# Kernel optimization log

Measured on AMD Instinct MI355X. Metric: run time of the kernel, lower is better.

## Reference

```python
import jax, jax.numpy as jnp
import numpy as np
import math

D_MODEL = 64
X_KS = 32   # input_kernel_size
Y_KS = 32   # output_kernel_size
HIDDEN = 256


def pos_enc(pos, d_model=D_MODEL):
    # standard interleaved sinusoidal encoding indexed by integer position
    i = jnp.arange(d_model // 2, dtype=jnp.float32)
    inv_freq = jnp.power(jnp.float32(10000.0), -(2.0 * i) / d_model)
    ang = pos.astype(jnp.float32)[:, None] * inv_freq[None, :]      # [N, d/2]
    pe = jnp.stack([jnp.sin(ang), jnp.cos(ang)], axis=-1)           # [N, d/2, 2]
    return pe.reshape(pos.shape[0], d_model)


def setup_inputs() -> dict:
    key = jax.random.key(0)
    ks = jax.random.split(key, 9)
    B, IN = 64, 1024
    d_in_w = 2 * D_MODEL + X_KS   # 160
    d_in_b = D_MODEL + Y_KS       # 96
    def lin(k, fan_in, fan_out):
        s = 1.0 / math.sqrt(fan_in)
        return jax.random.uniform(k, (fan_in, fan_out), jnp.float32, -s, s)
    return {
        "x": jax.random.normal(ks[0], (B, IN), jnp.float32),
        "output_size": 1024,
        "W1": lin(ks[1], d_in_w, HIDDEN), "b1": jnp.zeros((HIDDEN,), jnp.float32),
        "W2": lin(ks[2], HIDDEN, X_KS * Y_KS), "b2": jnp.zeros((X_KS * Y_KS,), jnp.float32),
        "Wb1": lin(ks[3], d_in_b, HIDDEN), "bb1": jnp.zeros((HIDDEN,), jnp.float32),
        "Wb2": lin(ks[4], HIDDEN, Y_KS), "bb2": jnp.zeros((Y_KS,), jnp.float32),
    }


def reference(x, output_size, W1, b1, W2, b2, Wb1, bb1, Wb2, bb2):
    B, input_size = x.shape
    gen_x = math.ceil(output_size / Y_KS)
    gen_y = math.ceil(input_size / X_KS)

    # pad x up to gen_y*X_KS and chunk into kernel windows, tiled gen_x times
    new_x = jnp.pad(x, ((0, 0), (0, gen_y * X_KS - input_size)))
    new_x = new_x.reshape(B, gen_y, X_KS)
    new_x = jnp.tile(new_x, (1, gen_x, 1))                          # [B, gx*gy, X_KS]

    arg_x = jnp.tile(jnp.arange(gen_x), gen_y)                      # [gx*gy]
    arg_y = jnp.repeat(jnp.arange(gen_y), gen_x)                    # [gx*gy]
    pe_x = jnp.broadcast_to(pos_enc(arg_x)[None], (B, gen_x * gen_y, D_MODEL))
    pe_y = jnp.broadcast_to(pos_enc(arg_y)[None], (B, gen_x * gen_y, D_MODEL))

    argument = jnp.concatenate([pe_x, pe_y, new_x], axis=2)         # [B, G, 2d+X_KS]

    # hypernetwork generates per-sample weight matrix
    h = jnp.tanh(argument @ W1 + b1)
    w = h @ W2 + b2                                                 # [B, G, X_KS*Y_KS]
    weight = w.reshape(B, gen_y * X_KS, gen_x * Y_KS)[:, :input_size, :output_size]

    out = jnp.einsum("bi,bio->bo", x, weight)                       # [B, output_size]

    # bias hypernetwork
    out_pad = jnp.pad(out, ((0, 0), (0, gen_x * Y_KS - output_size)))
    out_pad = out_pad.reshape(B, gen_x, Y_KS)
    pe_b = jnp.broadcast_to(pos_enc(jnp.arange(gen_x))[None], (B, gen_x, D_MODEL))
    hb = jnp.tanh(jnp.concatenate([out_pad, pe_b], axis=2) @ Wb1 + bb1)
    bias = (hb @ Wb2 + bb2).reshape(B, -1)[:, :output_size]

    return out + bias
```

## Files before the change

### kernel.cpp

```cpp
#include <hip/hip_runtime.h>
#include <math.h>

constexpr int B    = 64;
constexpr int IN   = 1024;
constexpr int OUTN = 1024;
constexpr int H    = 256;

#define LN10000 9.210340371976184f
#define TWO_LOG2E 2.8853900817779268f

__device__ __forceinline__ float fast_tanh(float x) {
    x = fminf(fmaxf(x, -15.0f), 15.0f);
    float e = __builtin_amdgcn_exp2f(x * TWO_LOG2E);
    return 1.0f - 2.0f * __builtin_amdgcn_rcpf(e + 1.0f);
}

__global__ void __launch_bounds__(512) k1_v(const float* __restrict__ x,
                                            const float* __restrict__ W1,
                                            const float* __restrict__ b1,
                                            float* __restrict__ v,
                                            float* __restrict__ S) {
    __shared__ float xs[1024];
    __shared__ float pe[32 * 64];
    __shared__ float A[32 * 64];
    __shared__ float Pyl[32 * 64];
    __shared__ float red[512];
    const int blk = blockIdx.x, tid = threadIdx.x;
    const int b = blk >> 2, cq = blk & 3, c0 = cq * 64;

    ((float2*)xs)[tid] = ((const float2*)(x + b * IN))[tid];
    #pragma unroll
    for (int r = 0; r < 2; ++r) {
        const int idx = r * 512 + tid;
        const int p = idx >> 5, i = idx & 31;
        float freq = expf(-(2.0f * (float)i / 64.0f) * LN10000);
        float a = (float)p * freq;
        pe[p * 64 + 2 * i]     = sinf(a);
        pe[p * 64 + 2 * i + 1] = cosf(a);
    }
    __syncthreads();

    if (cq == 0) {
        red[tid] = xs[tid] + xs[tid + 512];
        __syncthreads();
        for (int s = 256; s > 0; s >>= 1) {
            if (tid < s) red[tid] += red[tid + s];
            __syncthreads();
        }
        if (tid == 0) S[b] = red[0];
    }

    const int cl = tid & 63, jg = tid >> 6, j0 = jg * 4;
    const float b1v = b1[c0 + cl];
    float accA[4], accP[4];
    #pragma unroll
    for (int r = 0; r < 4; ++r) { accA[r] = b1v; accP[r] = 0.0f; }
    for (int d = 0; d < 64; ++d) {
        const float wx = W1[d * H + c0 + cl];
        const float wy = W1[(64 + d) * H + c0 + cl];
        #pragma unroll
        for (int r = 0; r < 4; ++r) {
            const float p = pe[(j0 + r) * 64 + d];
            accA[r] += p * wx;
            accP[r] += p * wy;
        }
    }
    for (int k = 0; k < 32; ++k) {
        const float wq = W1[(128 + k) * H + c0 + cl];
        #pragma unroll
        for (int r = 0; r < 4; ++r) accA[r] += xs[(j0 + r) * 32 + k] * wq;
    }
    #pragma unroll
    for (int r = 0; r < 4; ++r) {
        A[(j0 + r) * 64 + cl]   = accA[r];
        Pyl[(j0 + r) * 64 + cl] = accP[r];
    }
    __syncthreads();

    float Areg[32];
    #pragma unroll
    for (int jx = 0; jx < 32; ++jx) Areg[jx] = A[jx * 64 + cl];
    float acc = 0.0f;
    for (int r = 0; r < 4; ++r) {
        const int jy = j0 + r;
        const float pyv = Pyl[jy * 64 + cl];
        const float4* xr = (const float4*)(xs + jy * 32);
        #pragma unroll
        for (int q = 0; q < 8; ++q) {
            float4 xv = xr[q];
            acc += xv.x * fast_tanh(Areg[q * 4 + 0] + pyv);
            acc += xv.y * fast_tanh(Areg[q * 4 + 1] + pyv);
            acc += xv.z * fast_tanh(Areg[q * 4 + 2] + pyv);
            acc += xv.w * fast_tanh(Areg[q * 4 + 3] + pyv);
        }
    }
    red[tid] = acc;
    __syncthreads();
    if (tid < 64) {
        float s = 0.0f;
        #pragma unroll
        for (int g = 0; g < 8; ++g) s += red[g * 64 + tid];
        v[b * H + c0 + tid] = s;
    }
}

__global__ void __launch_bounds__(256) k2_out(const float* __restrict__ v,
                                              const float* __restrict__ S,
                                              const float* __restrict__ W2,
                                              const float* __restrict__ b2,
                                              const float* __restrict__ Wb1,
                                              const float* __restrict__ bb1,
                                              const float* __restrict__ Wb2,
                                              const float* __restrict__ bb2,
                                              float* __restrict__ out) {
    __shared__ float vsh[8 * 256];
    __shared__ float pes[64];
    __shared__ float hpe[256];
    __shared__ float os[8 * 32];
    __shared__ float hbs[8 * 256];
    __shared__ float Ssh[8];
    const int blk = blockIdx.x, tid = threadIdx.x;
    const int og = blk & 31, bg = blk >> 5;
    const int bl = tid >> 5, ol = tid & 31;
    const int b0 = bg * 8;

    ((float4*)vsh)[tid]       = ((const float4*)(v + b0 * H))[tid];
    ((float4*)vsh)[tid + 256] = ((const float4*)(v + b0 * H))[tid + 256];
    if (tid < 8) Ssh[tid] = S[b0 + tid];
    if (tid >= 64 && tid < 96) {
        const int i = tid - 64;
        float freq = expf(-(2.0f * (float)i / 64.0f) * LN10000);
        float a = (float)og * freq;
        pes[2 * i]     = sinf(a);
        pes[2 * i + 1] = cosf(a);
    }
    __syncthreads();

    {
        float a = bb1[tid];
        #pragma unroll 8
        for (int d = 0; d < 64; ++d)
            a += pes[d] * Wb1[(32 + d) * H + tid];
        hpe[tid] = a;
    }

    const int o = og * 32 + ol;
    float acc = Ssh[bl] * b2[o];
    const float4* vr = (const float4*)(vsh + bl * 256);
    #pragma unroll 4
    for (int c4 = 0; c4 < 64; ++c4) {
        float4 v4 = vr[c4];
        acc += v4.x * W2[(c4 * 4 + 0) * OUTN + o];
        acc += v4.y * W2[(c4 * 4 + 1) * OUTN + o];
        acc += v4.z * W2[(c4 * 4 + 2) * OUTN + o];
        acc += v4.w * W2[(c4 * 4 + 3) * OUTN + o];
    }
    os[bl * 32 + ol] = acc;
    __syncthreads();

    {
        const int c8 = ol * 8;
        float a[8];
        #pragma unroll
        for (int j = 0; j < 8; ++j) a[j] = hpe[c8 + j];
        #pragma unroll 4
        for (int k = 0; k < 32; ++k) {
            const float xo = os[bl * 32 + k];
            const float4* wr = (const float4*)(Wb1 + k * H + c8);
            float4 w0 = wr[0], w1 = wr[1];
            a[0] += xo * w0.x; a[1] += xo * w0.y; a[2] += xo * w0.z; a[3] += xo * w0.w;
            a[4] += xo * w1.x; a[5] += xo * w1.y; a[6] += xo * w1.z; a[7] += xo * w1.w;
        }
        #pragma unroll
        for (int j = 0; j < 8; ++j) hbs[bl * 256 + c8 + j] = fast_tanh(a[j]);
    }
    __syncthreads();

    {
        float bias = bb2[ol];
        const float4* hr = (const float4*)(hbs + bl * 256);
        #pragma unroll 4
        for (int c4 = 0; c4 < 64; ++c4) {
            float4 h4 = hr[c4];
            bias += h4.x * Wb2[(c4 * 4 + 0) * 32 + ol];
            bias += h4.y * Wb2[(c4 * 4 + 1) * 32 + ol];
            bias += h4.z * Wb2[(c4 * 4 + 2) * 32 + ol];
            bias += h4.w * Wb2[(c4 * 4 + 3) * 32 + ol];
        }
        out[(b0 + bl) * OUTN + og * 32 + ol] = os[bl * 32 + ol] + bias;
    }
}

extern "C" void kernel_launch(void* const* d_in, const int* in_sizes, int n_in,
                              void* d_out, int out_size, void* d_ws, size_t ws_size,
                              hipStream_t stream) {
    const float* x   = (const float*)d_in[0];
    const float* W1  = (const float*)d_in[2];
    const float* b1  = (const float*)d_in[3];
    const float* W2  = (const float*)d_in[4];
    const float* b2  = (const float*)d_in[5];
    const float* Wb1 = (const float*)d_in[6];
    const float* bb1 = (const float*)d_in[7];
    const float* Wb2 = (const float*)d_in[8];
    const float* bb2 = (const float*)d_in[9];
    float* out = (float*)d_out;

    float* v = (float*)d_ws;
    float* S = v + B * H;

    hipLaunchKernelGGL(k1_v,   dim3(B * 4), dim3(512), 0, stream, x, W1, b1, v, S);
    hipLaunchKernelGGL(k2_out, dim3(256),   dim3(256), 0, stream,
                       v, S, W2, b2, Wb1, bb1, Wb2, bb2, out);
}
```

Measured before the change: 103.1 us.

## Precompute positional-encoding tables in a prologue kernel and widen blocks to 1024 threads

Adds a small kernel that computes the batch-independent positional-encoding projections through W1, W1 (y part) and Wb1 once into workspace tables. The main kernels now run with 1024 threads per block. They read these tables instead of recomputing sin/cos and the 64-deep projections per block, and they split the W2 and Wb2 reductions across four thread groups with a shared-memory combine. This removes redundant per-block work and raises parallelism, at the cost of an extra kernel launch, more shared memory and extra syncs. The old path is kept as a fallback when the workspace is too small.

```diff
diff --git a/kernel.cpp b/kernel.cpp
--- a/kernel.cpp
+++ b/kernel.cpp
@@ -15,11 +15,197 @@
     return 1.0f - 2.0f * __builtin_amdgcn_rcpf(e + 1.0f);
 }
 
-__global__ void __launch_bounds__(512) k1_v(const float* __restrict__ x,
-                                            const float* __restrict__ W1,
-                                            const float* __restrict__ b1,
-                                            float* __restrict__ v,
-                                            float* __restrict__ S) {
+
+__global__ void __launch_bounds__(256) k0_tables(const float* __restrict__ W1,
+                                                 const float* __restrict__ b1,
+                                                 const float* __restrict__ Wb1,
+                                                 const float* __restrict__ bb1,
+                                                 float* __restrict__ PA,
+                                                 float* __restrict__ PY,
+                                                 float* __restrict__ HPE) {
+    __shared__ float pe[64];
+    const int blk = blockIdx.x, tid = threadIdx.x;
+    const int p = blk & 31, table = blk >> 5;
+    if (tid < 32) {
+        float freq = expf(-(2.0f * (float)tid / 64.0f) * LN10000);
+        float a = (float)p * freq;
+        pe[2 * tid]     = sinf(a);
+        pe[2 * tid + 1] = cosf(a);
+    }
+    __syncthreads();
+    const float* src; float bias; float* dst;
+    if (table == 0)      { src = W1;           bias = b1[tid];  dst = PA;  }
+    else if (table == 1) { src = W1 + 64 * H;  bias = 0.0f;     dst = PY;  }
+    else                 { src = Wb1 + 32 * H; bias = bb1[tid]; dst = HPE; }
+    float acc = bias;
+    #pragma unroll 16
+    for (int d = 0; d < 64; ++d) acc += pe[d] * src[d * H + tid];
+    dst[p * H + tid] = acc;
+}
+
+__global__ void __launch_bounds__(1024, 4) k1_new(const float* __restrict__ x,
+                                                  const float* __restrict__ W1,
+                                                  const float* __restrict__ PA,
+                                                  const float* __restrict__ PY,
+                                                  float* __restrict__ v,
+                                                  float* __restrict__ S) {
+    __shared__ float xs[1024];
+    __shared__ float w1s[2048];
+    __shared__ float As[2048];
+    __shared__ float Ps[2048];
+    __shared__ float red[1024];
+    const int blk = blockIdx.x, tid = threadIdx.x;
+    const int b = blk >> 2, cq = blk & 3, c0 = cq * 64;
+    const int cl = tid & 63, jg = tid >> 6;
+
+    xs[tid] = x[b * IN + tid];
+    #pragma unroll
+    for (int i = 0; i < 2; ++i) {
+        const int idx = i * 1024 + tid;
+        const int p = idx >> 6, c = idx & 63;
+        w1s[idx] = W1[(128 + p) * H + c0 + c];
+        Ps[idx]  = PY[p * H + c0 + c];
+    }
+    __syncthreads();
+
+    if (cq == 0 && tid < 64) {
+        float s = 0.0f;
+        #pragma unroll
+        for (int i = 0; i < 16; ++i) s += xs[tid + i * 64];
+        #pragma unroll
+        for (int off = 32; off > 0; off >>= 1) s += __shfl_xor(s, off, 64);
+        if (tid == 0) S[b] = s;
+    }
+
+    #pragma unroll
+    for (int r = 0; r < 2; ++r) {
+        const int jx = jg * 2 + r;
+        float q = PA[jx * H + c0 + cl];
+        #pragma unroll 8
+        for (int k = 0; k < 32; ++k)
+            q += xs[jx * 32 + k] * w1s[k * 64 + cl];
+        As[jx * 64 + cl] = q;
+    }
+    __syncthreads();
+
+    float Areg[32];
+    #pragma unroll
+    for (int jx = 0; jx < 32; ++jx) Areg[jx] = As[jx * 64 + cl];
+    float acc = 0.0f;
+    #pragma unroll
+    for (int r = 0; r < 2; ++r) {
+        const int jy = jg * 2 + r;
+        const float pyv = Ps[jy * 64 + cl];
+        const float4* xr = (const float4*)(xs + jy * 32);
+        #pragma unroll
+        for (int q8 = 0; q8 < 8; ++q8) {
+            float4 xv = xr[q8];
+            acc += xv.x * fast_tanh(Areg[q8 * 4 + 0] + pyv);
+            acc += xv.y * fast_tanh(Areg[q8 * 4 + 1] + pyv);
+            acc += xv.z * fast_tanh(Areg[q8 * 4 + 2] + pyv);
+            acc += xv.w * fast_tanh(Areg[q8 * 4 + 3] + pyv);
+        }
+    }
+    red[tid] = acc;
+    __syncthreads();
+    if (tid < 64) {
+        float s = 0.0f;
+        #pragma unroll
+        for (int g = 0; g < 16; ++g) s += red[g * 64 + tid];
+        v[b * H + c0 + tid] = s;
+    }
+}
+
+__global__ void __launch_bounds__(1024) k2_new(const float* __restrict__ v,
+                                               const float* __restrict__ S,
+                                               const float* __restrict__ W2,
+                                               const float* __restrict__ b2,
+                                               const float* __restrict__ Wb1,
+                                               const float* __restrict__ HPE,
+                                               const float* __restrict__ Wb2,
+                                               const float* __restrict__ bb2,
+                                               float* __restrict__ out) {
+    __shared__ float vsh[2048];
+    __shared__ float hpe[256];
+    __shared__ float osp[1024];
+    __shared__ float os[256];
+    __shared__ float hbs[2048];
+    __shared__ float Wb2s[8192];
+    __shared__ float bp[1024];
+    __shared__ float Ssh[8];
+    const int blk = blockIdx.x, tid = threadIdx.x;
+    const int og = blk & 31, bg = blk >> 5, b0 = bg * 8;
+    const int h = tid >> 8, u = tid & 255, bl = u >> 5, ol = u & 31;
+
+    ((float2*)vsh)[tid] = ((const float2*)(v + b0 * H))[tid];
+    #pragma unroll
+    for (int i = 0; i < 2; ++i)
+        ((float4*)Wb2s)[i * 1024 + tid] = ((const float4*)Wb2)[i * 1024 + tid];
+    if (tid < 256) hpe[tid] = HPE[og * H + tid];
+    if (tid < 8) Ssh[tid] = S[b0 + tid];
+    __syncthreads();
+
+    const int o = og * 32 + ol;
+    {
+        float acc = (h == 0) ? Ssh[bl] * b2[o] : 0.0f;
+        const float4* vr = (const float4*)(vsh + bl * H + h * 64);
+        const int cb = h * 64;
+        #pragma unroll
+        for (int c4 = 0; c4 < 16; ++c4) {
+            float4 v4 = vr[c4];
+            const int c = cb + c4 * 4;
+            acc += v4.x * W2[(c + 0) * OUTN + o];
+            acc += v4.y * W2[(c + 1) * OUTN + o];
+            acc += v4.z * W2[(c + 2) * OUTN + o];
+            acc += v4.w * W2[(c + 3) * OUTN + o];
+        }
+        osp[h * 256 + u] = acc;
+    }
+    __syncthreads();
+    if (tid < 256)
+        os[tid] = osp[tid] + osp[256 + tid] + osp[512 + tid] + osp[768 + tid];
+    __syncthreads();
+    {
+        float a0 = hpe[h * 64 + ol];
+        float a1 = hpe[h * 64 + 32 + ol];
+        #pragma unroll 8
+        for (int k = 0; k < 32; ++k) {
+            const float xo = os[bl * 32 + k];
+            const float* wr = Wb1 + k * H + h * 64 + ol;
+            a0 += xo * wr[0];
+            a1 += xo * wr[32];
+        }
+        hbs[bl * H + h * 64 + ol]      = fast_tanh(a0);
+        hbs[bl * H + h * 64 + 32 + ol] = fast_tanh(a1);
+    }
+    __syncthreads();
+    {
+        float bias = (h == 0) ? bb2[ol] : 0.0f;
+        const float4* hr = (const float4*)(hbs + bl * H + h * 64);
+        const int cb = h * 64;
+        #pragma unroll
+        for (int c4 = 0; c4 < 16; ++c4) {
+            float4 h4 = hr[c4];
+            const int c = cb + c4 * 4;
+            bias += h4.x * Wb2s[(c + 0) * 32 + ol];
+            bias += h4.y * Wb2s[(c + 1) * 32 + ol];
+            bias += h4.z * Wb2s[(c + 2) * 32 + ol];
+            bias += h4.w * Wb2s[(c + 3) * 32 + ol];
+        }
+        bp[h * 256 + u] = bias;
+    }
+    __syncthreads();
+    if (tid < 256) {
+        out[(b0 + (tid >> 5)) * OUTN + og * 32 + (tid & 31)] =
+            os[tid] + bp[tid] + bp[256 + tid] + bp[512 + tid] + bp[768 + tid];
+    }
+}
+
+__global__ void __launch_bounds__(512) k1_old(const float* __restrict__ x,
+                                              const float* __restrict__ W1,
+                                              const float* __restrict__ b1,
+                                              float* __restrict__ v,
+                                              float* __restrict__ S) {
     __shared__ float xs[1024];
     __shared__ float pe[32 * 64];
     __shared__ float A[32 * 64];
@@ -104,7 +290,7 @@
     }
 }
 
-__global__ void __launch_bounds__(256) k2_out(const float* __restrict__ v,
+__global__ void __launch_bounds__(256) k2_old(const float* __restrict__ v,
                                               const float* __restrict__ S,
                                               const float* __restrict__ W2,
                                               const float* __restrict__ b2,
@@ -208,7 +394,20 @@
     float* v = (float*)d_ws;
     float* S = v + B * H;
 
-    hipLaunchKernelGGL(k1_v,   dim3(B * 4), dim3(512), 0, stream, x, W1, b1, v, S);
-    hipLaunchKernelGGL(k2_out, dim3(256),   dim3(256), 0, stream,
-                       v, S, W2, b2, Wb1, bb1, Wb2, bb2, out);
-}
+    const size_t needA = (size_t)(B * H + B + 3 * 32 * H) * sizeof(float);
+    if (ws_size >= needA) {
+        float* PA  = S + B;
+        float* PY  = PA + 32 * H;
+        float* HPE = PY + 32 * H;
+        hipLaunchKernelGGL(k0_tables, dim3(96),  dim3(256),  0, stream,
+                           W1, b1, Wb1, bb1, PA, PY, HPE);
+        hipLaunchKernelGGL(k1_new,    dim3(B*4), dim3(1024), 0, stream,
+                           x, W1, PA, PY, v, S);
+        hipLaunchKernelGGL(k2_new,    dim3(256), dim3(1024), 0, stream,
+                           v, S, W2, b2, Wb1, HPE, Wb2, bb2, out);
+    } else {
+        hipLaunchKernelGGL(k1_old, dim3(B*4), dim3(512), 0, stream, x, W1, b1, v, S);
+        hipLaunchKernelGGL(k2_old, dim3(256), dim3(256), 0, stream,
+                           v, S, W2, b2, Wb1, bb1, Wb2, bb2, out);
+    }
+}
```

Result: faster. 90.96 us (-11.8%).

## Precompute positional-encoding tables once and widen k1/k2 to 1024 threads

Applied to the files above, without the earlier changes.

Adds a small pre-kernel that computes the positional-encoding projections through W1 (PA including b1, and PY) once, instead of every one of the 256 k1 blocks recomputing the full 32x64x64 pe products. k1 now uses 1024 threads, each holding one x element and broadcasting it through wavefront shuffles, with W1's x-rows kept in registers. k2 splits the hidden-dimension reductions across four thread groups with shared-memory partial sums to raise parallelism. The cost is an extra kernel launch, more workspace traffic, and extra synchronisation and reduction steps.

```diff
diff --git a/kernel.cpp b/kernel.cpp
--- a/kernel.cpp
+++ b/kernel.cpp
@@ -15,179 +15,180 @@
     return 1.0f - 2.0f * __builtin_amdgcn_rcpf(e + 1.0f);
 }
 
-__global__ void __launch_bounds__(512) k1_v(const float* __restrict__ x,
-                                            const float* __restrict__ W1,
-                                            const float* __restrict__ b1,
-                                            float* __restrict__ v,
-                                            float* __restrict__ S) {
-    __shared__ float xs[1024];
-    __shared__ float pe[32 * 64];
-    __shared__ float A[32 * 64];
-    __shared__ float Pyl[32 * 64];
-    __shared__ float red[512];
+__global__ void __launch_bounds__(256) k0_tables(const float* __restrict__ W1,
+                                                 const float* __restrict__ b1,
+                                                 float* __restrict__ PA,
+                                                 float* __restrict__ PY) {
+    __shared__ float pe[64];
+    const int blk = blockIdx.x, tid = threadIdx.x;
+    const int p = blk & 31, table = blk >> 5;
+    if (tid < 32) {
+        float freq = expf(-(2.0f * (float)tid / 64.0f) * LN10000);
+        float a = (float)p * freq;
+        pe[2 * tid]     = sinf(a);
+        pe[2 * tid + 1] = cosf(a);
+    }
+    __syncthreads();
+    const float* src = (table == 0) ? W1 : (W1 + 64 * H);
+    float acc = (table == 0) ? b1[tid] : 0.0f;
+    #pragma unroll 16
+    for (int d = 0; d < 64; ++d) acc += pe[d] * src[d * H + tid];
+    float* dst = (table == 0) ? PA : PY;
+    dst[p * H + tid] = acc;
+}
+
+__global__ void __launch_bounds__(1024, 4) k1_v(const float* __restrict__ x,
+                                                const float* __restrict__ W1,
+                                                const float* __restrict__ PA,
+                                                const float* __restrict__ PY,
+                                                float* __restrict__ v,
+                                                float* __restrict__ S) {
+    __shared__ float As[2048];
+    __shared__ float red[1024];
+    __shared__ float sred[16];
     const int blk = blockIdx.x, tid = threadIdx.x;
     const int b = blk >> 2, cq = blk & 3, c0 = cq * 64;
-
-    ((float2*)xs)[tid] = ((const float2*)(x + b * IN))[tid];
-    #pragma unroll
-    for (int r = 0; r < 2; ++r) {
-        const int idx = r * 512 + tid;
-        const int p = idx >> 5, i = idx & 31;
-        float freq = expf(-(2.0f * (float)i / 64.0f) * LN10000);
-        float a = (float)p * freq;
-        pe[p * 64 + 2 * i]     = sinf(a);
-        pe[p * 64 + 2 * i + 1] = cosf(a);
-    }
-    __syncthreads();
+    const int cl = tid & 63, jg = tid >> 6;
+    const int p0 = jg * 2;
+
+    const float xr = x[b * IN + tid];
+    float w1reg[32];
+    #pragma unroll
+    for (int k = 0; k < 32; ++k) w1reg[k] = W1[(128 + k) * H + c0 + cl];
+    float acc0 = PA[p0 * H + c0 + cl];
+    float acc1 = PA[(p0 + 1) * H + c0 + cl];
+    const float py0 = PY[p0 * H + c0 + cl];
+    const float py1 = PY[(p0 + 1) * H + c0 + cl];
 
     if (cq == 0) {
-        red[tid] = xs[tid] + xs[tid + 512];
-        __syncthreads();
-        for (int s = 256; s > 0; s >>= 1) {
-            if (tid < s) red[tid] += red[tid + s];
-            __syncthreads();
-        }
-        if (tid == 0) S[b] = red[0];
-    }
-
-    const int cl = tid & 63, jg = tid >> 6, j0 = jg * 4;
-    const float b1v = b1[c0 + cl];
-    float accA[4], accP[4];
-    #pragma unroll
-    for (int r = 0; r < 4; ++r) { accA[r] = b1v; accP[r] = 0.0f; }
-    for (int d = 0; d < 64; ++d) {
-        const float wx = W1[d * H + c0 + cl];
-        const float wy = W1[(64 + d) * H + c0 + cl];
-        #pragma unroll
-        for (int r = 0; r < 4; ++r) {
-            const float p = pe[(j0 + r) * 64 + d];
-            accA[r] += p * wx;
-            accP[r] += p * wy;
-        }
-    }
-    for (int k = 0; k < 32; ++k) {
-        const float wq = W1[(128 + k) * H + c0 + cl];
-        #pragma unroll
-        for (int r = 0; r < 4; ++r) accA[r] += xs[(j0 + r) * 32 + k] * wq;
-    }
-    #pragma unroll
-    for (int r = 0; r < 4; ++r) {
-        A[(j0 + r) * 64 + cl]   = accA[r];
-        Pyl[(j0 + r) * 64 + cl] = accP[r];
-    }
-    __syncthreads();
-
-    float Areg[32];
-    #pragma unroll
-    for (int jx = 0; jx < 32; ++jx) Areg[jx] = A[jx * 64 + cl];
+        float s = xr;
+        #pragma unroll
+        for (int off = 32; off > 0; off >>= 1) s += __shfl_xor(s, off, 64);
+        if (cl == 0) sred[jg] = s;
+    }
+
+    #pragma unroll
+    for (int k = 0; k < 32; ++k) acc0 += __shfl(xr, k, 64) * w1reg[k];
+    #pragma unroll
+    for (int k = 0; k < 32; ++k) acc1 += __shfl(xr, 32 + k, 64) * w1reg[k];
+
+    As[p0 * 64 + cl]       = acc0;
+    As[(p0 + 1) * 64 + cl] = acc1;
+    __syncthreads();
+
+    if (cq == 0 && tid == 0) {
+        float s = 0.0f;
+        #pragma unroll
+        for (int g = 0; g < 16; ++g) s += sred[g];
+        S[b] = s;
+    }
+
     float acc = 0.0f;
-    for (int r = 0; r < 4; ++r) {
-        const int jy = j0 + r;
-        const float pyv = Pyl[jy * 64 + cl];
-        const float4* xr = (const float4*)(xs + jy * 32);
-        #pragma unroll
-        for (int q = 0; q < 8; ++q) {
-            float4 xv = xr[q];
-            acc += xv.x * fast_tanh(Areg[q * 4 + 0] + pyv);
-            acc += xv.y * fast_tanh(Areg[q * 4 + 1] + pyv);
-            acc += xv.z * fast_tanh(Areg[q * 4 + 2] + pyv);
-            acc += xv.w * fast_tanh(Areg[q * 4 + 3] + pyv);
-        }
+    #pragma unroll
+    for (int jx = 0; jx < 32; ++jx) {
+        const float a = As[jx * 64 + cl];
+        acc += __shfl(xr, jx, 64)      * fast_tanh(a + py0);
+        acc += __shfl(xr, 32 + jx, 64) * fast_tanh(a + py1);
     }
     red[tid] = acc;
     __syncthreads();
     if (tid < 64) {
         float s = 0.0f;
         #pragma unroll
-        for (int g = 0; g < 8; ++g) s += red[g * 64 + tid];
+        for (int g = 0; g < 16; ++g) s += red[g * 64 + tid];
         v[b * H + c0 + tid] = s;
     }
 }
 
-__global__ void __launch_bounds__(256) k2_out(const float* __restrict__ v,
-                                              const float* __restrict__ S,
-                                              const float* __restrict__ W2,
-                                              const float* __restrict__ b2,
-                                              const float* __restrict__ Wb1,
-                                              const float* __restrict__ bb1,
-                                              const float* __restrict__ Wb2,
-                                              const float* __restrict__ bb2,
-                                              float* __restrict__ out) {
-    __shared__ float vsh[8 * 256];
-    __shared__ float pes[64];
+__global__ void __launch_bounds__(1024) k2_out(const float* __restrict__ v,
+                                               const float* __restrict__ S,
+                                               const float* __restrict__ W2,
+                                               const float* __restrict__ b2,
+                                               const float* __restrict__ Wb1,
+                                               const float* __restrict__ bb1,
+                                               const float* __restrict__ Wb2,
+                                               const float* __restrict__ bb2,
+                                               float* __restrict__ out) {
+    __shared__ float vsh[2048];
     __shared__ float hpe[256];
-    __shared__ float os[8 * 32];
-    __shared__ float hbs[8 * 256];
+    __shared__ float osp[1024];
+    __shared__ float os[256];
+    __shared__ float hbs[2048];
+    __shared__ float bp[1024];
     __shared__ float Ssh[8];
     const int blk = blockIdx.x, tid = threadIdx.x;
-    const int og = blk & 31, bg = blk >> 5;
-    const int bl = tid >> 5, ol = tid & 31;
-    const int b0 = bg * 8;
-
-    ((float4*)vsh)[tid]       = ((const float4*)(v + b0 * H))[tid];
-    ((float4*)vsh)[tid + 256] = ((const float4*)(v + b0 * H))[tid + 256];
+    const int og = blk & 31, bg = blk >> 5, b0 = bg * 8;
+    const int h = tid >> 8, u = tid & 255, bl = u >> 5, ol = u & 31;
+
+    ((float2*)vsh)[tid] = ((const float2*)(v + b0 * H))[tid];
     if (tid < 8) Ssh[tid] = S[b0 + tid];
-    if (tid >= 64 && tid < 96) {
-        const int i = tid - 64;
-        float freq = expf(-(2.0f * (float)i / 64.0f) * LN10000);
+    if (tid < 256) {
+        const int L = tid & 63;
+        float freq = expf(-(2.0f * (float)(L >> 1) / 64.0f) * LN10000);
         float a = (float)og * freq;
-        pes[2 * i]     = sinf(a);
-        pes[2 * i + 1] = cosf(a);
-    }
-    __syncthreads();
-
+        float pel = (L & 1) ? cosf(a) : sinf(a);
+        float accp = bb1[tid];
+        #pragma unroll 16
+        for (int d = 0; d < 64; ++d)
+            accp += __shfl(pel, d, 64) * Wb1[(32 + d) * H + tid];
+        hpe[tid] = accp;
+    }
+    __syncthreads();
+
+    const int o = og * 32 + ol;
     {
-        float a = bb1[tid];
-        #pragma unroll 8
-        for (int d = 0; d < 64; ++d)
-            a += pes[d] * Wb1[(32 + d) * H + tid];
-        hpe[tid] = a;
-    }
-
-    const int o = og * 32 + ol;
-    float acc = Ssh[bl] * b2[o];
-    const float4* vr = (const float4*)(vsh + bl * 256);
-    #pragma unroll 4
-    for (int c4 = 0; c4 < 64; ++c4) {
-        float4 v4 = vr[c4];
-        acc += v4.x * W2[(c4 * 4 + 0) * OUTN + o];
-        acc += v4.y * W2[(c4 * 4 + 1) * OUTN + o];
-        acc += v4.z * W2[(c4 * 4 + 2) * OUTN + o];
-        acc += v4.w * W2[(c4 * 4 + 3) * OUTN + o];
-    }
-    os[bl * 32 + ol] = acc;
-    __syncthreads();
-
+        float acc = (h == 0) ? Ssh[bl] * b2[o] : 0.0f;
+        const float4* vr = (const float4*)(vsh + bl * H + h * 64);
+        #pragma unroll
+        for (int c4 = 0; c4 < 16; ++c4) {
+            float4 v4 = vr[c4];
+            const int c = h * 64 + c4 * 4;
+            acc += v4.x * W2[(c + 0) * OUTN + o];
+            acc += v4.y * W2[(c + 1) * OUTN + o];
+            acc += v4.z * W2[(c + 2) * OUTN + o];
+            acc += v4.w * W2[(c + 3) * OUTN + o];
+        }
+        osp[h * 256 + u] = acc;
+    }
+    __syncthreads();
+    if (tid < 256)
+        os[tid] = osp[tid] + osp[256 + tid] + osp[512 + tid] + osp[768 + tid];
+    __syncthreads();
     {
-        const int c8 = ol * 8;
-        float a[8];
-        #pragma unroll
-        for (int j = 0; j < 8; ++j) a[j] = hpe[c8 + j];
-        #pragma unroll 4
-        for (int k = 0; k < 32; ++k) {
-            const float xo = os[bl * 32 + k];
-            const float4* wr = (const float4*)(Wb1 + k * H + c8);
-            float4 w0 = wr[0], w1 = wr[1];
-            a[0] += xo * w0.x; a[1] += xo * w0.y; a[2] += xo * w0.z; a[3] += xo * w0.w;
-            a[4] += xo * w1.x; a[5] += xo * w1.y; a[6] += xo * w1.z; a[7] += xo * w1.w;
+        float a0 = hpe[h * 64 + ol];
+        float a1 = hpe[h * 64 + 32 + ol];
+        const float4* osr = (const float4*)(os + bl * 32);
+        #pragma unroll
+        for (int k4 = 0; k4 < 8; ++k4) {
+            float4 o4 = osr[k4];
+            const float* wr = Wb1 + (k4 * 4) * H + h * 64 + ol;
+            a0 += o4.x * wr[0];         a1 += o4.x * wr[32];
+            a0 += o4.y * wr[H];         a1 += o4.y * wr[H + 32];
+            a0 += o4.z * wr[2 * H];     a1 += o4.z * wr[2 * H + 32];
+            a0 += o4.w * wr[3 * H];     a1 += o4.w * wr[3 * H + 32];
         }
-        #pragma unroll
-        for (int j = 0; j < 8; ++j) hbs[bl * 256 + c8 + j] = fast_tanh(a[j]);
-    }
-    __syncthreads();
-
+        hbs[bl * H + h * 64 + ol]      = fast_tanh(a0);
+        hbs[bl * H + h * 64 + 32 + ol] = fast_tanh(a1);
+    }
+    __syncthreads();
     {
-        float bias = bb2[ol];
-        const float4* hr = (const float4*)(hbs + bl * 256);
-        #pragma unroll 4
-        for (int c4 = 0; c4 < 64; ++c4) {
+        float bias = (h == 0) ? bb2[ol] : 0.0f;
+        const float4* hr = (const float4*)(hbs + bl * H + h * 64);
+        #pragma unroll
+        for (int c4 = 0; c4 < 16; ++c4) {
             float4 h4 = hr[c4];
-            bias += h4.x * Wb2[(c4 * 4 + 0) * 32 + ol];
-            bias += h4.y * Wb2[(c4 * 4 + 1) * 32 + ol];
-            bias += h4.z * Wb2[(c4 * 4 + 2) * 32 + ol];
-            bias += h4.w * Wb2[(c4 * 4 + 3) * 32 + ol];
+            const int c = h * 64 + c4 * 4;
+            bias += h4.x * Wb2[(c + 0) * 32 + ol];
+            bias += h4.y * Wb2[(c + 1) * 32 + ol];
+            bias += h4.z * Wb2[(c + 2) * 32 + ol];
+            bias += h4.w * Wb2[(c + 3) * 32 + ol];
         }
-        out[(b0 + bl) * OUTN + og * 32 + ol] = os[bl * 32 + ol] + bias;
+        bp[h * 256 + u] = bias;
+    }
+    __syncthreads();
+    if (tid < 256) {
+        out[(b0 + (tid >> 5)) * OUTN + og * 32 + (tid & 31)] =
+            os[tid] + bp[tid] + bp[256 + tid] + bp[512 + tid] + bp[768 + tid];
     }
 }
 
@@ -205,10 +206,13 @@
     const float* bb2 = (const float*)d_in[9];
     float* out = (float*)d_out;
 
-    float* v = (float*)d_ws;
-    float* S = v + B * H;
-
-    hipLaunchKernelGGL(k1_v,   dim3(B * 4), dim3(512), 0, stream, x, W1, b1, v, S);
-    hipLaunchKernelGGL(k2_out, dim3(256),   dim3(256), 0, stream,
+    float* v  = (float*)d_ws;
+    float* S  = v + B * H;
+    float* PA = S + B;
+    float* PY = PA + 32 * H;
+
+    hipLaunchKernelGGL(k0_tables, dim3(64),    dim3(256),  0, stream, W1, b1, PA, PY);
+    hipLaunchKernelGGL(k1_v,      dim3(B * 4), dim3(1024), 0, stream, x, W1, PA, PY, v, S);
+    hipLaunchKernelGGL(k2_out,    dim3(256),   dim3(1024), 0, stream,
                        v, S, W2, b2, Wb1, bb1, Wb2, bb2, out);
 }
```

Measured after the change: 92.88 us. 9.9% less time.
